# Performance work log

Hardware: AMD Instinct MI355X
Metric: run time of the kernel (lower is better)

The kernel has to match this reference:

```python
import jax, jax.numpy as jnp
import numpy as np

N, D, M, E, K = 16384, 512, 1024, 8, 2
LOSS_COEF = 0.01
EPS = 1e-10


def setup_inputs() -> dict:
    key = jax.random.key(0)
    ks = jax.random.split(key, 6)
    x = jax.random.normal(ks[0], (N, D), dtype=jnp.float32)
    # gate weight (torch init is zeros; use small random so routing is non-degenerate)
    w_gate = 0.02 * jax.random.normal(ks[1], (D, E), dtype=jnp.float32)
    # stacked expert FFN params: Linear(D->M), GELU, Linear(M->D)
    W1 = jax.random.normal(ks[2], (E, D, M), dtype=jnp.float32) / np.sqrt(D)
    b1 = jnp.zeros((E, M), dtype=jnp.float32)
    W2 = jax.random.normal(ks[3], (E, M, D), dtype=jnp.float32) / np.sqrt(M)
    b2 = jnp.zeros((E, D), dtype=jnp.float32)
    return {"x": x, "w_gate": w_gate, "W1": W1, "b1": b1, "W2": W2, "b2": b2}


def _cv_squared(v):
    # torch .var() is unbiased (ddof=1)
    v = v.astype(jnp.float32)
    return jnp.var(v, ddof=1) / (jnp.mean(v) ** 2 + EPS)


def reference(x, w_gate, W1, b1, W2, b2):
    n = x.shape[0]
    # --- noisy_top_k_gating (eval path: no noise) ---
    logits = x @ w_gate                                  # [N, E]
    top_logits, top_idx = jax.lax.top_k(logits, min(K + 1, E))
    topk_logits = top_logits[:, :K]                      # [N, K]
    topk_idx = top_idx[:, :K]                            # [N, K]
    topk_gates = jax.nn.softmax(topk_logits, axis=-1)    # [N, K]
    gates = jnp.zeros_like(logits).at[jnp.arange(n)[:, None], topk_idx].set(topk_gates)
    importance = gates.sum(axis=0)                       # [E]
    load = (gates > 0).sum(axis=0).astype(jnp.float32)   # [E]
    loss = LOSS_COEF * (_cv_squared(importance) + _cv_squared(load))
    # --- experts (dense equivalent of sparse dispatch/combine: gate==0 rows contribute 0) ---
    h = jnp.einsum('nd,edm->enm', x, W1) + b1[:, None, :]     # [E, N, M]
    h = jax.nn.gelu(h, approximate=False)
    out = jnp.einsum('enm,emd->end', h, W2) + b2[:, None, :]  # [E, N, D]
    y = jnp.einsum('ne,end->nd', gates, out)                  # [N, D]
    return (y, loss)
```

## Files before the change

### kernel.cpp

```cpp
#include <hip/hip_runtime.h>
#include <math.h>

#define NTOK 16384
#define DDIM 512
#define MDIM 1024
#define NEXP 8
#define BKW 32
#define TMAX 264

typedef __attribute__((ext_vector_type(8))) short short8;
typedef __attribute__((ext_vector_type(4))) float floatx4;

__device__ inline unsigned short f2bf(float f){
  union { float f; unsigned int u; } v; v.f = f;
  unsigned int u = v.u;
  u += ((u >> 16) & 1u) + 0x7fffu;
  return (unsigned short)(u >> 16);
}

__device__ inline float bf2f(unsigned short s){
  union { unsigned int u; float f; } v;
  v.u = ((unsigned int)s) << 16;
  return v.f;
}

__device__ inline float gelu_fast(float x){
  float u = x * 0.70710678118654752f;
  float a = fabsf(u);
  float t = __builtin_amdgcn_rcpf(fmaf(0.3275911f, a, 1.0f));
  float p = fmaf(1.061405429f, t, -1.453152027f);
  p = fmaf(p, t, 1.421413741f);
  p = fmaf(p, t, -0.284496736f);
  p = fmaf(p, t, 0.254829592f);
  p = p * t;
  float e = __expf(-u * u);
  float erfa = fmaf(-p, e, 1.0f);
  float erfu = copysignf(erfa, u);
  return 0.5f * x * (1.0f + erfu);
}

__device__ __forceinline__ void gload16(const unsigned short* g, unsigned short* l){
  __builtin_amdgcn_global_load_lds(
      (const __attribute__((address_space(1))) void*)g,
      (__attribute__((address_space(3))) void*)l,
      16, 0, 0);
}


__global__ void init_small_kernel(int* counts, float* imp){
  int t = threadIdx.x;
  if (t < NEXP){ counts[t] = 0; imp[t] = 0.0f; }
}

__global__ void transpose_conv_kernel(const float* __restrict__ in,
                                      unsigned short* __restrict__ out,
                                      int R, int C){
  __shared__ float tile[32][33];
  int e  = blockIdx.z;
  int c0 = blockIdx.x << 5;
  int r0 = blockIdx.y << 5;
  const float* src = in + (size_t)e * R * C;
  unsigned short* dst = out + (size_t)e * R * C;
  int tc = threadIdx.x;
  int tr = threadIdx.y;
  #pragma unroll
  for (int i = 0; i < 32; i += 8)
    tile[tr + i][tc] = src[(size_t)(r0 + tr + i) * C + c0 + tc];
  __syncthreads();
  #pragma unroll
  for (int i = 0; i < 32; i += 8)
    dst[(size_t)(c0 + tr + i) * R + r0 + tc] = f2bf(tile[tc][tr + i]);
}


__global__ __launch_bounds__(256)
void gating_kernel(const float* __restrict__ x,
                   const float* __restrict__ wg,
                   unsigned short* __restrict__ xb,
                   int* __restrict__ tok_e, float* __restrict__ tok_g,
                   int* __restrict__ counts, float* __restrict__ imp){
  __shared__ int   lcnt[NEXP];
  __shared__ float limp[NEXP];
  int t = threadIdx.x;
  if (t < NEXP){ lcnt[t] = 0; limp[t] = 0.0f; }
  __syncthreads();

  int wave = t >> 6;
  int lane = t & 63;

  for (int it = 0; it < 4; it++){
    int n = blockIdx.x * 16 + it * 4 + wave;

    const float4* xp = (const float4*)(x + (size_t)n * DDIM + lane * 8);
    float4 a = xp[0], b = xp[1];
    float xv[8] = {a.x, a.y, a.z, a.w, b.x, b.y, b.z, b.w};

    short8 xo;
    #pragma unroll
    for (int j = 0; j < 8; j++) xo[j] = (short)f2bf(xv[j]);
    *(short8*)(xb + (size_t)n * DDIM + lane * 8) = xo;

    double acc[NEXP];
    #pragma unroll
    for (int e = 0; e < NEXP; e++) acc[e] = 0.0;
    #pragma unroll
    for (int j = 0; j < 8; j++){
      const float* wr = wg + (size_t)(lane * 8 + j) * NEXP;
      #pragma unroll
      for (int e = 0; e < NEXP; e++) acc[e] += (double)xv[j] * (double)wr[e];
    }
    #pragma unroll
    for (int off = 32; off >= 1; off >>= 1){
      #pragma unroll
      for (int e = 0; e < NEXP; e++) acc[e] += __shfl_xor(acc[e], off);
    }
    if (lane == 0){
      int i0 = -1, i1 = -1;
      double l0 = -1e300, l1 = -1e300;
      #pragma unroll
      for (int e = 0; e < NEXP; e++){
        double v = acc[e];
        if (v > l0){ l1 = l0; i1 = i0; l0 = v; i0 = e; }
        else if (v > l1){ l1 = v; i1 = e; }
      }
      float ex = expf((float)(l1 - l0));
      float g0 = 1.0f / (1.0f + ex);
      float g1 = ex / (1.0f + ex);
      tok_e[n * 2]     = i0; tok_e[n * 2 + 1] = i1;
      tok_g[n * 2]     = g0; tok_g[n * 2 + 1] = g1;
      atomicAdd(&lcnt[i0], 1); atomicAdd(&lcnt[i1], 1);
      atomicAdd(&limp[i0], g0); atomicAdd(&limp[i1], g1);
    }
  }
  __syncthreads();
  if (t < NEXP){
    atomicAdd(&counts[t], lcnt[t]);
    atomicAdd(&imp[t], limp[t]);
  }
}

__global__ void loss_scan_kernel(const int* __restrict__ counts,
                                 const float* __restrict__ imp,
                                 int* __restrict__ offsets, int* __restrict__ cursor,
                                 int* __restrict__ tile_pre,
                                 float* __restrict__ out_loss){
  int off = 0, tp = 0;
  double si = 0, si2 = 0, sl = 0, sl2 = 0;
  for (int e = 0; e < NEXP; e++){
    offsets[e] = off; cursor[e] = off;
    tile_pre[e] = tp;
    tp += (counts[e] + 127) >> 7;
    off += counts[e];
    double im = (double)imp[e];
    double ld = (double)counts[e];
    si += im; si2 += im * im;
    sl += ld; sl2 += ld * ld;
  }
  offsets[NEXP] = off;
  tile_pre[NEXP] = tp;
  double mi = si / 8.0, ml = sl / 8.0;
  double vi = (si2 - 8.0 * mi * mi) / 7.0;
  double vl = (sl2 - 8.0 * ml * ml) / 7.0;
  double loss = 0.01 * (vi / (mi * mi + 1e-10) + vl / (ml * ml + 1e-10));
  *out_loss = (float)loss;
}

__global__ __launch_bounds__(256)
void scatter_kernel(const int* __restrict__ tok_e,
                    int* __restrict__ cursor,
                    int* __restrict__ btok, int* __restrict__ slot_of){
  __shared__ int lcnt[NEXP];
  __shared__ int lbase[NEXP];
  int t = threadIdx.x;
  if (t < NEXP) lcnt[t] = 0;
  __syncthreads();

  int n = blockIdx.x * 256 + t;
  int e0 = tok_e[n * 2], e1 = tok_e[n * 2 + 1];
  int r0 = atomicAdd(&lcnt[e0], 1);
  int r1 = atomicAdd(&lcnt[e1], 1);
  __syncthreads();
  if (t < NEXP) lbase[t] = atomicAdd(&cursor[t], lcnt[t]);
  __syncthreads();
  int s0 = lbase[e0] + r0;
  int s1 = lbase[e1] + r1;
  btok[s0] = n;
  btok[s1] = n;
  slot_of[n * 2]     = s0;
  slot_of[n * 2 + 1] = s1;
}


__global__ __launch_bounds__(256)
void gemm1_kernel(const unsigned short* __restrict__ xb,
                  const unsigned short* __restrict__ w1t,
                  const float* __restrict__ b1,
                  const int* __restrict__ offsets,
                  const int* __restrict__ tile_pre,
                  const int* __restrict__ btok,
                  unsigned short* __restrict__ H){
  int b = blockIdx.x;
  int L = (b & 7) * TMAX + (b >> 3);
  int ct = L & 7;
  int tt = L >> 3;
  if (tt >= tile_pre[NEXP]) return;
  int e = 0;
  while (tt >= tile_pre[e + 1]) e++;
  int rt = tt - tile_pre[e];
  int off = offsets[e];
  int cnt = offsets[e + 1] - off;
  int r0 = rt << 7;

  __shared__ unsigned short As[2 * 128 * BKW];
  __shared__ unsigned short Bs[2 * 128 * BKW];

  int t = threadIdx.x;
  int w = t >> 6;
  int l = t & 63;
  int lrow = l >> 2;
  int g = (l & 3) ^ ((l >> 3) & 3);

  const unsigned short* apt0;
  const unsigned short* apt1;
  {
    int ra0 = r0 + (0 * 4 + w) * 16 + lrow; if (ra0 >= cnt) ra0 = cnt - 1;
    int ra1 = r0 + (1 * 4 + w) * 16 + lrow; if (ra1 >= cnt) ra1 = cnt - 1;
    apt0 = xb + (size_t)btok[off + ra0] * DDIM + g * 8;
    apt1 = xb + (size_t)btok[off + ra1] * DDIM + g * 8;
  }
  const unsigned short* bpt0 = w1t + ((size_t)e * MDIM + (ct << 7) + w * 16 + lrow) * DDIM + g * 8;
  const unsigned short* bpt1 = bpt0 + (size_t)64 * DDIM;

  int lane = t & 63;
  int wr = (w >> 1) << 6;
  int wc = (w & 1) << 6;
  int lm = lane & 15;
  int lq = lane >> 4;
  int swz = (lm >> 1) & 3;

  int aoff[4], boff[4];
  #pragma unroll
  for (int i = 0; i < 4; i++){
    aoff[i] = (wr + i * 16 + lm) * BKW + ((lq ^ swz) << 3);
    boff[i] = (wc + i * 16 + lm) * BKW + ((lq ^ swz) << 3);
  }

  floatx4 acc[4][4] = {};

  #define STAGE1(K0, CB) {                                   \
    unsigned short* Ac = As + ((CB) << 12);                  \
    unsigned short* Bc = Bs + ((CB) << 12);                  \
    gload16(apt0 + (K0), Ac + w * 512);                      \
    gload16(apt1 + (K0), Ac + 2048 + w * 512);               \
    gload16(bpt0 + (K0), Bc + w * 512);                      \
    gload16(bpt1 + (K0), Bc + 2048 + w * 512);               \
  }
  #define COMPUTE1(CB) {                                     \
    const unsigned short* Ac = As + ((CB) << 12);            \
    const unsigned short* Bc = Bs + ((CB) << 12);            \
    short8 af[4], bfr[4];                                    \
    _Pragma("unroll")                                        \
    for (int i = 0; i < 4; i++) af[i]  = *(const short8*)(Ac + aoff[i]); \
    _Pragma("unroll")                                        \
    for (int j = 0; j < 4; j++) bfr[j] = *(const short8*)(Bc + boff[j]); \
    _Pragma("unroll")                                        \
    for (int i = 0; i < 4; i++)                              \
      _Pragma("unroll")                                      \
      for (int j = 0; j < 4; j++)                            \
        acc[i][j] = __builtin_amdgcn_mfma_f32_16x16x32_bf16(af[i], bfr[j], acc[i][j], 0, 0, 0); \
  }

  int cur = 0;
  STAGE1(0, 0);
  asm volatile("s_waitcnt vmcnt(0)" ::: "memory");
  __builtin_amdgcn_sched_barrier(0);
  __builtin_amdgcn_s_barrier();
  __builtin_amdgcn_sched_barrier(0);
  for (int k = 1; k < DDIM / BKW; k++){
    STAGE1(k * BKW, cur ^ 1);
    COMPUTE1(cur);
    asm volatile("s_waitcnt vmcnt(0)" ::: "memory");
    __builtin_amdgcn_sched_barrier(0);
    __builtin_amdgcn_s_barrier();
    __builtin_amdgcn_sched_barrier(0);
    cur ^= 1;
  }
  COMPUTE1(cur);
  #undef STAGE1
  #undef COMPUTE1

  const float* bias = b1 + e * MDIM + (ct << 7);
  #pragma unroll
  for (int i = 0; i < 4; i++){
    int rbase = wr + i * 16 + lq * 4;
    #pragma unroll
    for (int j = 0; j < 4; j++){
      int cc = wc + j * 16 + lm;
      float bv = bias[cc];
      #pragma unroll
      for (int r = 0; r < 4; r++){
        int row = r0 + rbase + r;
        if (row < cnt){
          float v = acc[i][j][r] + bv;
          H[(size_t)(off + row) * MDIM + (ct << 7) + cc] = f2bf(gelu_fast(v));
        }
      }
    }
  }
}

__global__ __launch_bounds__(256)
void gemm2_kernel(const unsigned short* __restrict__ H,
                  const unsigned short* __restrict__ w2t,
                  const float* __restrict__ b2,
                  const int* __restrict__ offsets,
                  const int* __restrict__ tile_pre,
                  unsigned short* __restrict__ O){
  int b = blockIdx.x;
  int L = (b & 7) * (TMAX / 2) + (b >> 3);
  int ct = L & 3;
  int tt = L >> 2;
  if (tt >= tile_pre[NEXP]) return;
  int e = 0;
  while (tt >= tile_pre[e + 1]) e++;
  int rt = tt - tile_pre[e];
  int off = offsets[e];
  int cnt = offsets[e + 1] - off;
  int r0 = rt << 7;

  __shared__ unsigned short As[2 * 128 * BKW];
  __shared__ unsigned short Bs[2 * 128 * BKW];

  int t = threadIdx.x;
  int w = t >> 6;
  int l = t & 63;
  int lrow = l >> 2;
  int g = (l & 3) ^ ((l >> 3) & 3);

  const unsigned short* apt0;
  const unsigned short* apt1;
  {
    int ra0 = r0 + w * 16 + lrow;        if (ra0 >= cnt) ra0 = cnt - 1;
    int ra1 = r0 + 64 + w * 16 + lrow;   if (ra1 >= cnt) ra1 = cnt - 1;
    apt0 = H + (size_t)(off + ra0) * MDIM + g * 8;
    apt1 = H + (size_t)(off + ra1) * MDIM + g * 8;
  }
  const unsigned short* bpt0 = w2t + ((size_t)e * DDIM + (ct << 7) + w * 16 + lrow) * MDIM + g * 8;
  const unsigned short* bpt1 = bpt0 + (size_t)64 * MDIM;

  int lane = t & 63;
  int wr = (w >> 1) << 6;
  int wc = (w & 1) << 6;
  int lm = lane & 15;
  int lq = lane >> 4;
  int swz = (lm >> 1) & 3;

  int aoff[4], boff[4];
  #pragma unroll
  for (int i = 0; i < 4; i++){
    aoff[i] = (wr + i * 16 + lm) * BKW + ((lq ^ swz) << 3);
    boff[i] = (wc + i * 16 + lm) * BKW + ((lq ^ swz) << 3);
  }

  floatx4 acc[4][4] = {};

  #define STAGE2(K0, CB) {                                   \
    unsigned short* Ac = As + ((CB) << 12);                  \
    unsigned short* Bc = Bs + ((CB) << 12);                  \
    gload16(apt0 + (K0), Ac + w * 512);                      \
    gload16(apt1 + (K0), Ac + 2048 + w * 512);               \
    gload16(bpt0 + (K0), Bc + w * 512);                      \
    gload16(bpt1 + (K0), Bc + 2048 + w * 512);               \
  }
  #define COMPUTE2(CB) {                                     \
    const unsigned short* Ac = As + ((CB) << 12);            \
    const unsigned short* Bc = Bs + ((CB) << 12);            \
    short8 af[4], bfr[4];                                    \
    _Pragma("unroll")                                        \
    for (int i = 0; i < 4; i++) af[i]  = *(const short8*)(Ac + aoff[i]); \
    _Pragma("unroll")                                        \
    for (int j = 0; j < 4; j++) bfr[j] = *(const short8*)(Bc + boff[j]); \
    _Pragma("unroll")                                        \
    for (int i = 0; i < 4; i++)                              \
      _Pragma("unroll")                                      \
      for (int j = 0; j < 4; j++)                            \
        acc[i][j] = __builtin_amdgcn_mfma_f32_16x16x32_bf16(af[i], bfr[j], acc[i][j], 0, 0, 0); \
  }

  int cur = 0;
  STAGE2(0, 0);
  asm volatile("s_waitcnt vmcnt(0)" ::: "memory");
  __builtin_amdgcn_sched_barrier(0);
  __builtin_amdgcn_s_barrier();
  __builtin_amdgcn_sched_barrier(0);
  for (int k = 1; k < MDIM / BKW; k++){
    STAGE2(k * BKW, cur ^ 1);
    COMPUTE2(cur);
    asm volatile("s_waitcnt vmcnt(0)" ::: "memory");
    __builtin_amdgcn_sched_barrier(0);
    __builtin_amdgcn_s_barrier();
    __builtin_amdgcn_sched_barrier(0);
    cur ^= 1;
  }
  COMPUTE2(cur);
  #undef STAGE2
  #undef COMPUTE2

  const float* bias = b2 + e * DDIM + (ct << 7);
  #pragma unroll
  for (int i = 0; i < 4; i++){
    int rbase = wr + i * 16 + lq * 4;
    #pragma unroll
    for (int j = 0; j < 4; j++){
      int cc = wc + j * 16 + lm;
      float bv = bias[cc];
      #pragma unroll
      for (int r = 0; r < 4; r++){
        int row = r0 + rbase + r;
        if (row < cnt)
          O[(size_t)(off + row) * DDIM + (ct << 7) + cc] = f2bf(acc[i][j][r] + bv);
      }
    }
  }
}


__global__ __launch_bounds__(256)
void combine_kernel(const unsigned short* __restrict__ O,
                    const float* __restrict__ tok_g,
                    const int* __restrict__ slot_of,
                    float* __restrict__ y){
  int wave = threadIdx.x >> 6;
  int lane = threadIdx.x & 63;
  int n = blockIdx.x * 4 + wave;
  int s0 = slot_of[n * 2], s1 = slot_of[n * 2 + 1];
  float g0 = tok_g[n * 2], g1 = tok_g[n * 2 + 1];
  short8 a = *(const short8*)(O + (size_t)s0 * DDIM + lane * 8);
  short8 b = *(const short8*)(O + (size_t)s1 * DDIM + lane * 8);
  float4 o0, o1;
  float* po0 = (float*)&o0;
  float* po1 = (float*)&o1;
  #pragma unroll
  for (int j = 0; j < 4; j++){
    po0[j] = g0 * bf2f((unsigned short)a[j]) + g1 * bf2f((unsigned short)b[j]);
    po1[j] = g0 * bf2f((unsigned short)a[j + 4]) + g1 * bf2f((unsigned short)b[j + 4]);
  }
  float4* yp = (float4*)(y + (size_t)n * DDIM + lane * 8);
  yp[0] = o0;
  yp[1] = o1;
}


extern "C" void kernel_launch(void* const* d_in, const int* in_sizes, int n_in,
                              void* d_out, int out_size, void* d_ws, size_t ws_size,
                              hipStream_t stream){
  const float* x  = (const float*)d_in[0];
  const float* wg = (const float*)d_in[1];
  const float* W1 = (const float*)d_in[2];
  const float* b1 = (const float*)d_in[3];
  const float* W2 = (const float*)d_in[4];
  const float* b2 = (const float*)d_in[5];
  float* y = (float*)d_out;

  char* ws = (char*)d_ws;
  size_t o = 0;
  auto alloc = [&](size_t bytes)->char*{
    char* p = ws + o;
    o += (bytes + 255) & ~(size_t)255;
    return p;
  };
  unsigned short* xb   = (unsigned short*)alloc((size_t)NTOK * DDIM * 2);
  unsigned short* w1t  = (unsigned short*)alloc((size_t)NEXP * MDIM * DDIM * 2);
  unsigned short* w2t  = (unsigned short*)alloc((size_t)NEXP * DDIM * MDIM * 2);
  unsigned short* H    = (unsigned short*)alloc((size_t)NTOK * 2 * MDIM * 2);
  unsigned short* O    = (unsigned short*)alloc((size_t)NTOK * 2 * DDIM * 2);
  int*   btok    = (int*)  alloc((size_t)NTOK * 2 * 4);
  int*   slot_of = (int*)  alloc((size_t)NTOK * 2 * 4);
  int*   tok_e   = (int*)  alloc((size_t)NTOK * 2 * 4);
  float* tok_g   = (float*)alloc((size_t)NTOK * 2 * 4);
  int*   counts  = (int*)  alloc(64);
  float* imp     = (float*)alloc(64);
  int*   offsets = (int*)  alloc(64);
  int*   cursor  = (int*)  alloc(64);
  int*   tile_pre= (int*)  alloc(64);

  hipLaunchKernelGGL(init_small_kernel, dim3(1), dim3(64), 0, stream, counts, imp);
  hipLaunchKernelGGL(transpose_conv_kernel, dim3(MDIM / 32, DDIM / 32, NEXP), dim3(32, 8), 0, stream,
                     W1, w1t, DDIM, MDIM);
  hipLaunchKernelGGL(transpose_conv_kernel, dim3(DDIM / 32, MDIM / 32, NEXP), dim3(32, 8), 0, stream,
                     W2, w2t, MDIM, DDIM);
  hipLaunchKernelGGL(gating_kernel, dim3(NTOK / 16), dim3(256), 0, stream,
                     x, wg, xb, tok_e, tok_g, counts, imp);
  hipLaunchKernelGGL(loss_scan_kernel, dim3(1), dim3(1), 0, stream,
                     counts, imp, offsets, cursor, tile_pre, y + (size_t)NTOK * DDIM);
  hipLaunchKernelGGL(scatter_kernel, dim3(NTOK / 256), dim3(256), 0, stream,
                     tok_e, cursor, btok, slot_of);
  hipLaunchKernelGGL(gemm1_kernel, dim3(TMAX * 8), dim3(256), 0, stream,
                     xb, w1t, b1, offsets, tile_pre, btok, H);
  hipLaunchKernelGGL(gemm2_kernel, dim3(TMAX * 4), dim3(256), 0, stream,
                     H, w2t, b2, offsets, tile_pre, O);
  hipLaunchKernelGGL(combine_kernel, dim3(NTOK / 4), dim3(256), 0, stream,
                     O, tok_g, slot_of, y);
}
```

Measured before the change: 303.1 us.

## Triple-buffer LDS tiles in both expert GEMMs with prefetch distance two

Both expert GEMM kernels move from double to triple-buffered shared-memory staging. Global loads are issued two K-steps ahead, and the wait is relaxed to vmcnt(4), so each barrier waits only for the older stage rather than draining all loads. The aim is to hide global-load latency behind MFMA work. In exchange, LDS per block grows by half, which may lower occupancy. The GEMM1 row-index expression is also rewritten into an equivalent form.

```diff
diff --git a/kernel.cpp b/kernel.cpp
--- a/kernel.cpp
+++ b/kernel.cpp
@@ -211,8 +211,8 @@
   int cnt = offsets[e + 1] - off;
   int r0 = rt << 7;
 
-  __shared__ unsigned short As[2 * 128 * BKW];
-  __shared__ unsigned short Bs[2 * 128 * BKW];
+  __shared__ unsigned short As[3 * 128 * BKW];
+  __shared__ unsigned short Bs[3 * 128 * BKW];
 
   int t = threadIdx.x;
   int w = t >> 6;
@@ -223,8 +223,8 @@
   const unsigned short* apt0;
   const unsigned short* apt1;
   {
-    int ra0 = r0 + (0 * 4 + w) * 16 + lrow; if (ra0 >= cnt) ra0 = cnt - 1;
-    int ra1 = r0 + (1 * 4 + w) * 16 + lrow; if (ra1 >= cnt) ra1 = cnt - 1;
+    int ra0 = r0 + w * 16 + lrow;        if (ra0 >= cnt) ra0 = cnt - 1;
+    int ra1 = r0 + 64 + w * 16 + lrow;   if (ra1 >= cnt) ra1 = cnt - 1;
     apt0 = xb + (size_t)btok[off + ra0] * DDIM + g * 8;
     apt1 = xb + (size_t)btok[off + ra1] * DDIM + g * 8;
   }
@@ -248,46 +248,65 @@
   floatx4 acc[4][4] = {};
 
   #define STAGE1(K0, CB) {                                   \
-    unsigned short* Ac = As + ((CB) << 12);                  \
-    unsigned short* Bc = Bs + ((CB) << 12);                  \
+    unsigned short* Ac = As + (CB) * 4096;                   \
+    unsigned short* Bc = Bs + (CB) * 4096;                   \
     gload16(apt0 + (K0), Ac + w * 512);                      \
     gload16(apt1 + (K0), Ac + 2048 + w * 512);               \
     gload16(bpt0 + (K0), Bc + w * 512);                      \
     gload16(bpt1 + (K0), Bc + 2048 + w * 512);               \
   }
-  #define COMPUTE1(CB) {                                     \
-    const unsigned short* Ac = As + ((CB) << 12);            \
-    const unsigned short* Bc = Bs + ((CB) << 12);            \
-    short8 af[4], bfr[4];                                    \
+  #define READ1(CB) {                                        \
+    const unsigned short* Ac = As + (CB) * 4096;             \
+    const unsigned short* Bc = Bs + (CB) * 4096;             \
     _Pragma("unroll")                                        \
     for (int i = 0; i < 4; i++) af[i]  = *(const short8*)(Ac + aoff[i]); \
     _Pragma("unroll")                                        \
     for (int j = 0; j < 4; j++) bfr[j] = *(const short8*)(Bc + boff[j]); \
+  }
+  #define MFMA1 {                                            \
     _Pragma("unroll")                                        \
     for (int i = 0; i < 4; i++)                              \
       _Pragma("unroll")                                      \
       for (int j = 0; j < 4; j++)                            \
         acc[i][j] = __builtin_amdgcn_mfma_f32_16x16x32_bf16(af[i], bfr[j], acc[i][j], 0, 0, 0); \
   }
-
+  #define WAITBAR(N) {                                       \
+    asm volatile("s_waitcnt vmcnt(" #N ")" ::: "memory");    \
+    __builtin_amdgcn_sched_barrier(0);                       \
+    __builtin_amdgcn_s_barrier();                            \
+    __builtin_amdgcn_sched_barrier(0);                       \
+  }
+
+  const int NK = DDIM / BKW;
+  STAGE1(0, 0);
+  STAGE1(BKW, 1);
+  WAITBAR(4);
   int cur = 0;
-  STAGE1(0, 0);
-  asm volatile("s_waitcnt vmcnt(0)" ::: "memory");
-  __builtin_amdgcn_sched_barrier(0);
-  __builtin_amdgcn_s_barrier();
-  __builtin_amdgcn_sched_barrier(0);
-  for (int k = 1; k < DDIM / BKW; k++){
-    STAGE1(k * BKW, cur ^ 1);
-    COMPUTE1(cur);
-    asm volatile("s_waitcnt vmcnt(0)" ::: "memory");
-    __builtin_amdgcn_sched_barrier(0);
-    __builtin_amdgcn_s_barrier();
-    __builtin_amdgcn_sched_barrier(0);
-    cur ^= 1;
-  }
-  COMPUTE1(cur);
+  for (int k = 0; k < NK - 2; k++){
+    int st = cur + 2; if (st >= 3) st -= 3;
+    short8 af[4], bfr[4];
+    READ1(cur);
+    STAGE1((k + 2) * BKW, st);
+    MFMA1;
+    WAITBAR(4);
+    cur = (cur + 1 == 3) ? 0 : cur + 1;
+  }
+  {
+    short8 af[4], bfr[4];
+    READ1(cur);
+    MFMA1;
+    WAITBAR(0);
+    cur = (cur + 1 == 3) ? 0 : cur + 1;
+  }
+  {
+    short8 af[4], bfr[4];
+    READ1(cur);
+    MFMA1;
+  }
   #undef STAGE1
-  #undef COMPUTE1
+  #undef READ1
+  #undef MFMA1
+  #undef WAITBAR
 
   const float* bias = b1 + e * MDIM + (ct << 7);
   #pragma unroll
@@ -328,8 +347,8 @@
   int cnt = offsets[e + 1] - off;
   int r0 = rt << 7;
 
-  __shared__ unsigned short As[2 * 128 * BKW];
-  __shared__ unsigned short Bs[2 * 128 * BKW];
+  __shared__ unsigned short As[3 * 128 * BKW];
+  __shared__ unsigned short Bs[3 * 128 * BKW];
 
   int t = threadIdx.x;
   int w = t >> 6;
@@ -365,46 +384,65 @@
   floatx4 acc[4][4] = {};
 
   #define STAGE2(K0, CB) {                                   \
-    unsigned short* Ac = As + ((CB) << 12);                  \
-    unsigned short* Bc = Bs + ((CB) << 12);                  \
+    unsigned short* Ac = As + (CB) * 4096;                   \
+    unsigned short* Bc = Bs + (CB) * 4096;                   \
     gload16(apt0 + (K0), Ac + w * 512);                      \
     gload16(apt1 + (K0), Ac + 2048 + w * 512);               \
     gload16(bpt0 + (K0), Bc + w * 512);                      \
     gload16(bpt1 + (K0), Bc + 2048 + w * 512);               \
   }
-  #define COMPUTE2(CB) {                                     \
-    const unsigned short* Ac = As + ((CB) << 12);            \
-    const unsigned short* Bc = Bs + ((CB) << 12);            \
-    short8 af[4], bfr[4];                                    \
+  #define READ2(CB) {                                        \
+    const unsigned short* Ac = As + (CB) * 4096;             \
+    const unsigned short* Bc = Bs + (CB) * 4096;             \
     _Pragma("unroll")                                        \
     for (int i = 0; i < 4; i++) af[i]  = *(const short8*)(Ac + aoff[i]); \
     _Pragma("unroll")                                        \
     for (int j = 0; j < 4; j++) bfr[j] = *(const short8*)(Bc + boff[j]); \
+  }
+  #define MFMA2 {                                            \
     _Pragma("unroll")                                        \
     for (int i = 0; i < 4; i++)                              \
       _Pragma("unroll")                                      \
       for (int j = 0; j < 4; j++)                            \
         acc[i][j] = __builtin_amdgcn_mfma_f32_16x16x32_bf16(af[i], bfr[j], acc[i][j], 0, 0, 0); \
   }
-
+  #define WAITBAR2(N) {                                      \
+    asm volatile("s_waitcnt vmcnt(" #N ")" ::: "memory");    \
+    __builtin_amdgcn_sched_barrier(0);                       \
+    __builtin_amdgcn_s_barrier();                            \
+    __builtin_amdgcn_sched_barrier(0);                       \
+  }
+
+  const int NK = MDIM / BKW;
+  STAGE2(0, 0);
+  STAGE2(BKW, 1);
+  WAITBAR2(4);
   int cur = 0;
-  STAGE2(0, 0);
-  asm volatile("s_waitcnt vmcnt(0)" ::: "memory");
-  __builtin_amdgcn_sched_barrier(0);
-  __builtin_amdgcn_s_barrier();
-  __builtin_amdgcn_sched_barrier(0);
-  for (int k = 1; k < MDIM / BKW; k++){
-    STAGE2(k * BKW, cur ^ 1);
-    COMPUTE2(cur);
-    asm volatile("s_waitcnt vmcnt(0)" ::: "memory");
-    __builtin_amdgcn_sched_barrier(0);
-    __builtin_amdgcn_s_barrier();
-    __builtin_amdgcn_sched_barrier(0);
-    cur ^= 1;
-  }
-  COMPUTE2(cur);
+  for (int k = 0; k < NK - 2; k++){
+    int st = cur + 2; if (st >= 3) st -= 3;
+    short8 af[4], bfr[4];
+    READ2(cur);
+    STAGE2((k + 2) * BKW, st);
+    MFMA2;
+    WAITBAR2(4);
+    cur = (cur + 1 == 3) ? 0 : cur + 1;
+  }
+  {
+    short8 af[4], bfr[4];
+    READ2(cur);
+    MFMA2;
+    WAITBAR2(0);
+    cur = (cur + 1 == 3) ? 0 : cur + 1;
+  }
+  {
+    short8 af[4], bfr[4];
+    READ2(cur);
+    MFMA2;
+  }
   #undef STAGE2
-  #undef COMPUTE2
+  #undef READ2
+  #undef MFMA2
+  #undef WAITBAR2
 
   const float* bias = b2 + e * DDIM + (ct << 7);
   #pragma unroll
```

Result: faster. 285.0 us (-6.0%).
